# Kernel tuning notes

Measured on AMD Instinct MI355X. Metric: run time of the kernel, lower is better.

## Reference

```python
import jax, jax.numpy as jnp
import numpy as np

EPS = 1e-5

def conv3x3(x, w, b, stride=1):
    y = jax.lax.conv_general_dilated(x, w, (stride, stride), 'SAME',
                                     dimension_numbers=('NCHW', 'OIHW', 'NCHW'))
    return y + b[None, :, None, None]

def batchnorm_train(x, gamma, beta):
    # training-mode BN: batch statistics over (N, H, W)
    mean = x.mean(axis=(0, 2, 3), keepdims=True)
    var = x.var(axis=(0, 2, 3), keepdims=True)
    xh = (x - mean) * jax.lax.rsqrt(var + EPS)
    return xh * gamma[None, :, None, None] + beta[None, :, None, None]

def haar_dwt2(x):
    # pywt.dwt2(x, 'db1') on last two axes; even H,W so 'symmetric' padding is a no-op.
    # a = (x0 + x1)/sqrt2, d = (x0 - x1)/sqrt2 per axis -> 2x2 block combinations / 2.
    x00 = x[:, :, 0::2, 0::2]
    x01 = x[:, :, 0::2, 1::2]
    x10 = x[:, :, 1::2, 0::2]
    x11 = x[:, :, 1::2, 1::2]
    cA = (x00 + x01 + x10 + x11) * 0.5
    cH = (x00 + x01 - x10 - x11) * 0.5  # pywt 'da': detail along rows
    cV = (x00 - x01 + x10 - x11) * 0.5  # pywt 'ad': detail along cols
    cD = (x00 - x01 - x10 + x11) * 0.5
    return cA, cH, cV, cD


def setup_inputs() -> dict:
    key = jax.random.key(0)
    ks = jax.random.split(key, 8)
    N, in_c, out_c, H, W = 4, 3, 64, 512, 512

    def kaiming(k, shape):
        fan_in = shape[1] * shape[2] * shape[3]
        return jax.random.normal(k, shape, jnp.float32) * np.sqrt(2.0 / fan_in)

    inputs = jax.random.normal(ks[0], (N, in_c, H, W), jnp.float32)
    return {
        'inputs': inputs,
        # conv_block: conv1 -> bn1 -> conv2 -> bn2 -> relu
        'w1': kaiming(ks[1], (out_c, in_c, 3, 3)),
        'b1': jnp.zeros((out_c,), jnp.float32),
        'g1': jnp.ones((out_c,), jnp.float32),
        'be1': jnp.zeros((out_c,), jnp.float32),
        'w2': kaiming(ks[2], (out_c, out_c, 3, 3)),
        'b2': jnp.zeros((out_c,), jnp.float32),
        'g2': jnp.ones((out_c,), jnp.float32),
        'be2': jnp.zeros((out_c,), jnp.float32),
        # conv_dwt_block: conv(out_c*4 -> out_c) -> bn -> relu
        'w3': kaiming(ks[3], (out_c, out_c * 4, 3, 3)),
        'b3': jnp.zeros((out_c,), jnp.float32),
        'g3': jnp.ones((out_c,), jnp.float32),
        'be3': jnp.zeros((out_c,), jnp.float32),
    }


def reference(inputs, w1, b1, g1, be1, w2, b2, g2, be2, w3, b3, g3, be3):
    # conv_block
    x = conv3x3(inputs, w1, b1)
    x = batchnorm_train(x, g1, be1)
    x = conv3x3(x, w2, b2)
    x = batchnorm_train(x, g2, be2)
    skip_con = jax.nn.relu(x)

    # original detaches skip_con before the (CPU pywt) DWT -> no grad through this branch
    dwt_in = jax.lax.stop_gradient(skip_con)
    cA, cH, cV, cD = haar_dwt2(dwt_in)
    dwt = jnp.concatenate((cA, cH, cV, cD), axis=1)  # [N, 4*out_c, H/2, W/2]

    y = conv3x3(dwt, w3, b3)
    y = batchnorm_train(y, g3, be3)
    dwt_out = jax.nn.relu(y)
    return dwt_out, skip_con
```

## Files before the change

### kernel.cpp

```cpp
#include <hip/hip_runtime.h>
#include <cstdint>

typedef float f32x4 __attribute__((ext_vector_type(4)));
typedef __bf16 bf16x8 __attribute__((ext_vector_type(8)));
typedef unsigned int uint32;
typedef unsigned short ushort_t;

__device__ __forceinline__ ushort_t f2bf(float f) {
    uint32 u = __builtin_bit_cast(uint32, f);
    u = (u + 0x7fffu + ((u >> 16) & 1u)) >> 16;
    return (ushort_t)u;
}
__device__ __forceinline__ float bf2f(ushort_t h) {
    return __builtin_bit_cast(float, (uint32)h << 16);
}

__global__ __launch_bounds__(256) void im2col1_kernel(
    const float* __restrict__ in,
    ushort_t* __restrict__ P)
{
    int px = blockIdx.x * 256 + threadIdx.x;
    int n = px >> 18, rem = px & 262143;
    int y = rem >> 9, x = rem & 511;
    ushort_t pv[32];
#pragma unroll
    for (int ci = 0; ci < 3; ++ci)
#pragma unroll
        for (int t = 0; t < 9; ++t) {
            int dy = t / 3 - 1, dx = t % 3 - 1;
            int yy = y + dy, xx = x + dx;
            bool v = ((unsigned)yy < 512u) && ((unsigned)xx < 512u);
            pv[ci * 9 + t] = v ? f2bf(in[((n * 3 + ci) * 512 + yy) * 512 + xx])
                               : (ushort_t)0;
        }
#pragma unroll
    for (int k = 27; k < 32; ++k) pv[k] = 0;
    uint4* dst = (uint4*)(P + (size_t)px * 32);
    dst[0] = *(uint4*)(pv);
    dst[1] = *(uint4*)(pv + 8);
    dst[2] = *(uint4*)(pv + 16);
    dst[3] = *(uint4*)(pv + 24);
}

__global__ void prepw1_kernel(const float* __restrict__ w1,
                              ushort_t* __restrict__ Wsw1)
{
    int i = blockIdx.x * 256 + threadIdx.x;
    int ii = i & 7, lane = (i >> 3) & 63, nt = i >> 9;
    int cout = nt * 16 + (lane & 15);
    int k = (lane >> 4) * 8 + ii;
    Wsw1[i] = (k < 27) ? f2bf(w1[cout * 27 + k]) : (ushort_t)0;
}

__global__ __launch_bounds__(256) void gemm1_kernel(
    const ushort_t* __restrict__ P,
    const ushort_t* __restrict__ Wsw1,
    const float* __restrict__ b1,
    ushort_t* __restrict__ X1,
    float* __restrict__ stats)
{
    __shared__ float sred[4][128];
    int tid = threadIdx.x;
    int wave = tid >> 6, lane = tid & 63;
    int lp = lane & 15, lg = lane >> 4;
    int pxb = blockIdx.x * 256 + wave * 64;

    bf16x8 wf[4];
#pragma unroll
    for (int nt = 0; nt < 4; ++nt)
        wf[nt] = *(const bf16x8*)(Wsw1 + (nt * 64 + lane) * 8);

    f32x4 acc[4][4];
#pragma unroll
    for (int a = 0; a < 4; ++a)
#pragma unroll
        for (int b = 0; b < 4; ++b) acc[a][b] = (f32x4){0.f, 0.f, 0.f, 0.f};

#pragma unroll
    for (int nf = 0; nf < 4; ++nf) {
        bf16x8 bfrag = *(const bf16x8*)(P + (size_t)(pxb + nf * 16 + lp) * 32 + lg * 8);
#pragma unroll
        for (int nt = 0; nt < 4; ++nt)
            acc[nt][nf] = __builtin_amdgcn_mfma_f32_16x16x32_bf16(
                wf[nt], bfrag, acc[nt][nf], 0, 0, 0);
    }

    float s16[16], q16[16];
#pragma unroll
    for (int j = 0; j < 16; ++j) { s16[j] = 0.f; q16[j] = 0.f; }

#pragma unroll
    for (int nf = 0; nf < 4; ++nf) {
        size_t px = (size_t)pxb + nf * 16 + lp;
#pragma unroll
        for (int nt = 0; nt < 4; ++nt) {
            ushort_t ov[4];
#pragma unroll
            for (int r = 0; r < 4; ++r) {
                float o = acc[nt][nf][r] + b1[nt * 16 + lg * 4 + r];
                s16[nt * 4 + r] += o;
                q16[nt * 4 + r] += o * o;
                ov[r] = f2bf(o);
            }
            *(ushort4*)(X1 + px * 64 + nt * 16 + lg * 4) = *(ushort4*)ov;
        }
    }

#pragma unroll
    for (int off = 1; off < 16; off <<= 1)
#pragma unroll
        for (int j = 0; j < 16; ++j) {
            s16[j] += __shfl_xor(s16[j], off);
            q16[j] += __shfl_xor(q16[j], off);
        }
    if (lp == 0) {
#pragma unroll
        for (int nt = 0; nt < 4; ++nt)
#pragma unroll
            for (int r = 0; r < 4; ++r) {
                int ch = nt * 16 + lg * 4 + r;
                sred[wave][ch]      = s16[nt * 4 + r];
                sred[wave][64 + ch] = q16[nt * 4 + r];
            }
    }
    __syncthreads();
    if (tid < 128) {
        float tot = sred[0][tid] + sred[1][tid] + sred[2][tid] + sred[3][tid];
        atomicAdd(&stats[(blockIdx.x & 31) * 128 + tid], tot);
    }
}

__global__ void finalize_kernel(const float* __restrict__ stats,
                                const float* __restrict__ gamma,
                                const float* __restrict__ beta,
                                float inv_cnt, float* __restrict__ scsh)
{
    int c = threadIdx.x;
    float S = 0.f, Q = 0.f;
    for (int b = 0; b < 32; ++b) {
        S += stats[b * 128 + c];
        Q += stats[b * 128 + 64 + c];
    }
    float mean = S * inv_cnt;
    float var  = Q * inv_cnt - mean * mean;
    float rs   = rsqrtf(var + 1e-5f);
    float sc   = gamma[c] * rs;
    scsh[c]      = sc;
    scsh[64 + c] = beta[c] - mean * sc;
}

__global__ __launch_bounds__(256) void prepw_kernel(
    const float* __restrict__ w, const float* __restrict__ scale,
    ushort_t* __restrict__ Wsw, int CIN)
{
    int i = blockIdx.x * 256 + threadIdx.x;
    int KC = CIN >> 5;
    int ii = i & 7, lane = (i >> 3) & 63, nt = (i >> 9) & 3;
    int rest = i >> 11;
    int kc = rest % KC, t = rest / KC;
    if (t >= 9) return;
    int cout = nt * 16 + (lane & 15);
    int cin  = kc * 32 + (lane >> 4) * 8 + ii;
    float v = w[(cout * CIN + cin) * 9 + t];
    if (scale) v *= scale[cin];
    Wsw[i] = f2bf(v);
}

__global__ void prepT_kernel(const float* __restrict__ w2,
                             const float* __restrict__ shift,
                             float* __restrict__ T)
{
    int idx = threadIdx.x;
    if (idx < 576) {
        int t = idx / 64, cout = idx % 64;
        float s = 0.f;
        for (int cin = 0; cin < 64; ++cin)
            s += w2[(cout * 64 + cin) * 9 + t] * shift[cin];
        T[idx] = s;
    }
    __syncthreads();
    if (idx < 64) {
        float s = 0.f;
        for (int t = 0; t < 9; ++t) s += T[t * 64 + idx];
        T[576 + idx] = s;
    }
}

template <int CIN, bool HAS_T, int HH, int WW, int TILES>
__global__ __launch_bounds__(256, 3) void conv_mfma3_kernel(
    const ushort_t* __restrict__ X,
    const ushort_t* __restrict__ Wsw,
    const float* __restrict__ T,
    const float* __restrict__ bias,
    ushort_t* __restrict__ Y,
    float* __restrict__ stats)
{
    constexpr int KC     = CIN >> 5;
    constexpr int STAGES = TILES * KC;
    constexpr int CSTR   = WW / (64 * TILES);
    constexpr int RSTR   = HH >> 2;
    constexpr int NLD    = 1584;

    __shared__ ushort_t lds0[12672];
    __shared__ ushort_t lds1[12672];
    __shared__ float sred[4][128];

    int nwg = gridDim.x;
    int bid = blockIdx.x;
    int cpx = nwg >> 3;
    int bs  = (bid & 7) * cpx + (bid >> 3);

    int tid  = threadIdx.x;
    int wave = tid >> 6, lane = tid & 63;
    int lp = lane & 15, lg = lane >> 4;

    int tmp = bs;
    int cs = tmp % CSTR;  tmp /= CSTR;
    int rs = tmp % RSTR;
    int n  = tmp / RSTR;
    int y0 = rs << 2, x0 = cs * (64 * TILES);
    int y  = y0 + wave;

    for (int i = tid; i < 512; i += 256) ((float*)sred)[i] = 0.f;

    f32x4 acc[4][4];
#pragma unroll
    for (int a = 0; a < 4; ++a)
#pragma unroll
        for (int b = 0; b < 4; ++b) acc[a][b] = (f32x4){0.f, 0.f, 0.f, 0.f};

    uint4 rbuf[7];

    auto issue_stage = [&](int s) {
        int tj = s / KC, c = s - tj * KC;
        int xt = x0 + tj * 64;
#pragma unroll
        for (int j = 0; j < 7; ++j) {
            int idx = tid + j * 256;
            uint4 v = {0u, 0u, 0u, 0u};
            if (idx < NLD) {
                int p  = idx >> 2;
                int ry = p / 66, cx = p - ry * 66;
                int gy = y0 - 1 + ry, gx = xt - 1 + cx;
                if (((unsigned)gy < (unsigned)HH) && ((unsigned)gx < (unsigned)WW))
                    v = *(const uint4*)(X + ((size_t)(n * HH + gy) * WW + gx) * CIN
                                          + c * 32 + (idx & 3) * 8);
            }
            rbuf[j] = v;
        }
    };
    auto write_stage = [&](ushort_t* buf) {
#pragma unroll
        for (int j = 0; j < 7; ++j) {
            int idx = tid + j * 256;
            if (idx < NLD) ((uint4*)buf)[idx] = rbuf[j];
        }
    };

    issue_stage(0);
    write_stage(lds0);
    __syncthreads();

    ushort_t* cur = lds0;
    ushort_t* nxt = lds1;

#pragma unroll 1
    for (int s = 0; s < STAGES; ++s) {
        int tj = s / KC, c = s - tj * KC;
        if (s + 1 < STAGES) issue_stage(s + 1);

#pragma unroll
        for (int t = 0; t < 9; ++t) {
            const int dy = t / 3 - 1, dx = t % 3 - 1;
            bf16x8 wf[4];
#pragma unroll
            for (int nt = 0; nt < 4; ++nt)
                wf[nt] = *(const bf16x8*)(Wsw + (size_t)(((t * KC + c) << 2) + nt) * 512 + lane * 8);
            int prow = (wave + 1 + dy) * 66 + (1 + dx) + lp;
#pragma unroll
            for (int nf = 0; nf < 4; ++nf) {
                int px = prow + nf * 16;
                bf16x8 bfrag = *(const bf16x8*)((const char*)cur + px * 64 + lg * 16);
#pragma unroll
                for (int nt = 0; nt < 4; ++nt)
                    acc[nt][nf] = __builtin_amdgcn_mfma_f32_16x16x32_bf16(
                        wf[nt], bfrag, acc[nt][nf], 0, 0, 0);
            }
        }

        if (c == KC - 1) {
            int xt = x0 + tj * 64;
            bool top = (y == 0), bot = (y == HH - 1);
            float s16[16], q16[16];
            size_t rowbase = ((size_t)(n * HH + y) * WW) * 64;
#pragma unroll
            for (int nf = 0; nf < 4; ++nf) {
                int x = xt + nf * 16 + lp;
                bool lft = (x == 0), rgt = (x == WW - 1);
                bool edge = top | bot | lft | rgt;
#pragma unroll
                for (int nt = 0; nt < 4; ++nt) {
                    ushort_t ov[4];
#pragma unroll
                    for (int r = 0; r < 4; ++r) {
                        int ch = nt * 16 + lg * 4 + r;
                        float o = acc[nt][nf][r] + bias[ch];
                        if (HAS_T) {
                            o += T[576 + ch];
                            if (edge) {
#pragma unroll
                                for (int t = 0; t < 9; ++t) {
                                    int dy = t / 3 - 1, dx = t % 3 - 1;
                                    bool miss = (top && dy < 0) || (bot && dy > 0) ||
                                                (lft && dx < 0) || (rgt && dx > 0);
                                    if (miss) o -= T[t * 64 + ch];
                                }
                            }
                        }
                        if (nf == 0) { s16[nt * 4 + r] = o; q16[nt * 4 + r] = o * o; }
                        else         { s16[nt * 4 + r] += o; q16[nt * 4 + r] += o * o; }
                        ov[r] = f2bf(o);
                    }
                    *(ushort4*)(Y + rowbase + (size_t)x * 64 + nt * 16 + lg * 4) = *(ushort4*)ov;
                }
            }
#pragma unroll
            for (int off = 1; off < 16; off <<= 1)
#pragma unroll
                for (int j = 0; j < 16; ++j) {
                    s16[j] += __shfl_xor(s16[j], off);
                    q16[j] += __shfl_xor(q16[j], off);
                }
            if (lp == 0) {
#pragma unroll
                for (int nt = 0; nt < 4; ++nt)
#pragma unroll
                    for (int r = 0; r < 4; ++r) {
                        int ch = nt * 16 + lg * 4 + r;
                        sred[wave][ch]      += s16[nt * 4 + r];
                        sred[wave][64 + ch] += q16[nt * 4 + r];
                    }
            }
#pragma unroll
            for (int a = 0; a < 4; ++a)
#pragma unroll
                for (int b = 0; b < 4; ++b) acc[a][b] = (f32x4){0.f, 0.f, 0.f, 0.f};
        }

        if (s + 1 < STAGES) write_stage(nxt);
        __syncthreads();
        ushort_t* t2 = cur; cur = nxt; nxt = t2;
    }

    if (tid < 128) {
        float tot = sred[0][tid] + sred[1][tid] + sred[2][tid] + sred[3][tid];
        atomicAdd(&stats[(bs & 31) * 128 + tid], tot);
    }
}

__global__ __launch_bounds__(256) void bn2_dwt_skip_kernel(
    const ushort_t* __restrict__ X2, const float* __restrict__ scsh,
    float* __restrict__ skip,
    ushort_t* __restrict__ X3)
{
    __shared__ float v[128][65];
    int tid = threadIdx.x;
    int b = blockIdx.x;
    int n  = b >> 11;
    int r2 = b & 2047;
    int y0 = (r2 >> 3) << 1;
    int x0 = (r2 & 7) << 6;

#pragma unroll
    for (int k = 0; k < 4; ++k) {
        int q  = tid + k * 256;
        int px = q >> 3;
        int cb = (q & 7) * 8;
        int gy = y0 + (px >> 6);
        int gx = x0 + (px & 63);
        uint4 raw = *(const uint4*)(X2 + ((size_t)(n * 512 + gy) * 512 + gx) * 64 + cb);
        const ushort_t* up = (const ushort_t*)&raw;
#pragma unroll
        for (int j = 0; j < 8; ++j) {
            float f = bf2f(up[j]);
            float o = f * scsh[cb + j] + scsh[64 + cb + j];
            v[px][cb + j] = fmaxf(o, 0.f);
        }
    }
    __syncthreads();

    {
        int c = tid >> 2, sub = tid & 3;
#pragma unroll
        for (int rr = 0; rr < 2; ++rr) {
            float* orow = skip + ((size_t)(n * 64 + c) * 512 + (y0 + rr)) * 512 + x0;
#pragma unroll
            for (int qq = 0; qq < 4; ++qq) {
                int xb = qq * 16 + sub * 4;
                float4 w4;
                w4.x = v[rr * 64 + xb + 0][c];
                w4.y = v[rr * 64 + xb + 1][c];
                w4.z = v[rr * 64 + xb + 2][c];
                w4.w = v[rr * 64 + xb + 3][c];
                *(float4*)(orow + xb) = w4;
            }
        }
    }
    {
        int c = tid & 63, jj = tid >> 6;
        int yq = y0 >> 1, xq = x0 >> 1;
#pragma unroll
        for (int it = 0; it < 8; ++it) {
            int xl = jj * 8 + it;
            float x00 = v[2 * xl][c],      x01 = v[2 * xl + 1][c];
            float x10 = v[64 + 2 * xl][c], x11 = v[64 + 2 * xl + 1][c];
            float cA = (x00 + x01 + x10 + x11) * 0.5f;
            float cH = (x00 + x01 - x10 - x11) * 0.5f;
            float cV = (x00 - x01 + x10 - x11) * 0.5f;
            float cD = (x00 - x01 - x10 + x11) * 0.5f;
            ushort_t* dst = X3 + ((size_t)(n * 256 + yq) * 256 + xq + xl) * 256 + c;
            dst[0]   = f2bf(cA);
            dst[64]  = f2bf(cH);
            dst[128] = f2bf(cV);
            dst[192] = f2bf(cD);
        }
    }
}

__global__ __launch_bounds__(256) void bn3_kernel(
    const ushort_t* __restrict__ X4, const float* __restrict__ scsh,
    float* __restrict__ out)
{
    __shared__ float v[64][65];
    int tid = threadIdx.x;
    int b = blockIdx.x;
    int n  = b >> 10;
    int r2 = b & 1023;
    int y  = r2 >> 2;
    int x0 = (r2 & 3) << 6;

#pragma unroll
    for (int k = 0; k < 2; ++k) {
        int q  = tid + k * 256;
        int px = q >> 3;
        int cb = (q & 7) * 8;
        uint4 raw = *(const uint4*)(X4 + ((size_t)(n * 256 + y) * 256 + x0 + px) * 64 + cb);
        const ushort_t* up = (const ushort_t*)&raw;
#pragma unroll
        for (int j = 0; j < 8; ++j) {
            float f = bf2f(up[j]);
            float o = f * scsh[cb + j] + scsh[64 + cb + j];
            v[px][cb + j] = fmaxf(o, 0.f);
        }
    }
    __syncthreads();
    int c = tid >> 2, sub = tid & 3;
    float* orow = out + ((size_t)(n * 64 + c) * 256 + y) * 256 + x0;
#pragma unroll
    for (int qq = 0; qq < 4; ++qq) {
        int xb = qq * 16 + sub * 4;
        float4 w4;
        w4.x = v[xb + 0][c];
        w4.y = v[xb + 1][c];
        w4.z = v[xb + 2][c];
        w4.w = v[xb + 3][c];
        *(float4*)(orow + xb) = w4;
    }
}

extern "C" void kernel_launch(void* const* d_in, const int* in_sizes, int n_in,
                              void* d_out, int out_size, void* d_ws, size_t ws_size,
                              hipStream_t stream)
{
    const float* in  = (const float*)d_in[0];
    const float* w1  = (const float*)d_in[1];
    const float* b1  = (const float*)d_in[2];
    const float* g1  = (const float*)d_in[3];
    const float* be1 = (const float*)d_in[4];
    const float* w2  = (const float*)d_in[5];
    const float* b2  = (const float*)d_in[6];
    const float* g2  = (const float*)d_in[7];
    const float* be2 = (const float*)d_in[8];
    const float* w3  = (const float*)d_in[9];
    const float* b3  = (const float*)d_in[10];
    const float* g3  = (const float*)d_in[11];
    const float* be3 = (const float*)d_in[12];

    float* out     = (float*)d_out;
    float* dwt_out = out;
    float* skip    = out + 16777216;

    char* ws = (char*)d_ws;
    ushort_t* X1 = (ushort_t*)ws;
    ushort_t* X2 = (ushort_t*)(ws + 134217728);
    ushort_t* P  = X2;
    ushort_t* X3 = X1;
    ushort_t* X4 = X2;
    char* aux = ws + 268435456;
    float* stats1 = (float*)(aux);
    float* stats2 = (float*)(aux + 16384);
    float* stats3 = (float*)(aux + 32768);
    float* scsh1  = (float*)(aux + 49152);
    float* scsh2  = (float*)(aux + 49664);
    float* scsh3  = (float*)(aux + 50176);
    float* T2     = (float*)(aux + 50688);
    ushort_t* Wsw2 = (ushort_t*)(aux + 57344);
    ushort_t* Wsw3 = (ushort_t*)(aux + 131072);
    ushort_t* Wsw1 = (ushort_t*)(aux + 425984);

    hipMemsetAsync(aux, 0, 49152, stream);

    im2col1_kernel<<<4096, 256, 0, stream>>>(in, P);
    prepw1_kernel<<<8, 256, 0, stream>>>(w1, Wsw1);
    gemm1_kernel<<<4096, 256, 0, stream>>>(P, Wsw1, b1, X1, stats1);
    finalize_kernel<<<1, 64, 0, stream>>>(stats1, g1, be1, 1.f / 1048576.f, scsh1);
    prepw_kernel<<<144, 256, 0, stream>>>(w2, scsh1, Wsw2, 64);
    prepT_kernel<<<1, 576, 0, stream>>>(w2, scsh1 + 64, T2);

    conv_mfma3_kernel<64, true, 512, 512, 4><<<1024, 256, 0, stream>>>(
        X1, Wsw2, T2, b2, X2, stats2);
    finalize_kernel<<<1, 64, 0, stream>>>(stats2, g2, be2, 1.f / 1048576.f, scsh2);

    bn2_dwt_skip_kernel<<<8192, 256, 0, stream>>>(X2, scsh2, skip, X3);

    prepw_kernel<<<576, 256, 0, stream>>>(w3, nullptr, Wsw3, 256);
    conv_mfma3_kernel<256, false, 256, 256, 1><<<1024, 256, 0, stream>>>(
        X3, Wsw3, nullptr, b3, X4, stats3);
    finalize_kernel<<<1, 64, 0, stream>>>(stats3, g3, be3, 1.f / 262144.f, scsh3);

    bn3_kernel<<<4096, 256, 0, stream>>>(X4, scsh3, dwt_out);
}
```

Baseline: 620.5 us.

## Replace double-buffered multi-tile conv with single-buffer per-tile kernel

```diff
diff --git a/kernel.cpp b/kernel.cpp
--- a/kernel.cpp
+++ b/kernel.cpp
@@ -186,8 +186,8 @@
     }
 }
 
-template <int CIN, bool HAS_T, int HH, int WW, int TILES>
-__global__ __launch_bounds__(256, 3) void conv_mfma3_kernel(
+template <int CIN, bool HAS_T, int HH, int WW>
+__global__ __launch_bounds__(256, 4) void conv_mfma4_kernel(
     const ushort_t* __restrict__ X,
     const ushort_t* __restrict__ Wsw,
     const float* __restrict__ T,
@@ -196,13 +196,10 @@
     float* __restrict__ stats)
 {
     constexpr int KC     = CIN >> 5;
-    constexpr int STAGES = TILES * KC;
-    constexpr int CSTR   = WW / (64 * TILES);
-    constexpr int RSTR   = HH >> 2;
-    constexpr int NLD    = 1584;
-
-    __shared__ ushort_t lds0[12672];
-    __shared__ ushort_t lds1[12672];
+    constexpr int COLS_B = WW >> 6;
+    constexpr int ROWS_B = HH >> 2;
+
+    __shared__ ushort_t tile[12672];
     __shared__ float sred[4][128];
 
     int nwg = gridDim.x;
@@ -215,59 +212,36 @@
     int lp = lane & 15, lg = lane >> 4;
 
     int tmp = bs;
-    int cs = tmp % CSTR;  tmp /= CSTR;
-    int rs = tmp % RSTR;
-    int n  = tmp / RSTR;
-    int y0 = rs << 2, x0 = cs * (64 * TILES);
+    int ctile = tmp % COLS_B;  tmp /= COLS_B;
+    int rtile = tmp % ROWS_B;
+    int n     = tmp / ROWS_B;
+    int y0 = rtile << 2, x0 = ctile << 6;
     int y  = y0 + wave;
 
-    for (int i = tid; i < 512; i += 256) ((float*)sred)[i] = 0.f;
-
     f32x4 acc[4][4];
 #pragma unroll
     for (int a = 0; a < 4; ++a)
 #pragma unroll
         for (int b = 0; b < 4; ++b) acc[a][b] = (f32x4){0.f, 0.f, 0.f, 0.f};
 
-    uint4 rbuf[7];
-
-    auto issue_stage = [&](int s) {
-        int tj = s / KC, c = s - tj * KC;
-        int xt = x0 + tj * 64;
+#pragma unroll 1
+    for (int c = 0; c < KC; ++c) {
+        if (c) __syncthreads();
 #pragma unroll
         for (int j = 0; j < 7; ++j) {
-            int idx = tid + j * 256;
-            uint4 v = {0u, 0u, 0u, 0u};
-            if (idx < NLD) {
-                int p  = idx >> 2;
-                int ry = p / 66, cx = p - ry * 66;
-                int gy = y0 - 1 + ry, gx = xt - 1 + cx;
+            int s = tid + j * 256;
+            if (s < 1584) {
+                int px = s >> 2, cb = s & 3;
+                int ry = px / 66, cx = px - ry * 66;
+                int gy = y0 - 1 + ry, gx = x0 - 1 + cx;
+                uint4 v = {0u, 0u, 0u, 0u};
                 if (((unsigned)gy < (unsigned)HH) && ((unsigned)gx < (unsigned)WW))
                     v = *(const uint4*)(X + ((size_t)(n * HH + gy) * WW + gx) * CIN
-                                          + c * 32 + (idx & 3) * 8);
-            }
-            rbuf[j] = v;
-        }
-    };
-    auto write_stage = [&](ushort_t* buf) {
-#pragma unroll
-        for (int j = 0; j < 7; ++j) {
-            int idx = tid + j * 256;
-            if (idx < NLD) ((uint4*)buf)[idx] = rbuf[j];
-        }
-    };
-
-    issue_stage(0);
-    write_stage(lds0);
-    __syncthreads();
-
-    ushort_t* cur = lds0;
-    ushort_t* nxt = lds1;
-
-#pragma unroll 1
-    for (int s = 0; s < STAGES; ++s) {
-        int tj = s / KC, c = s - tj * KC;
-        if (s + 1 < STAGES) issue_stage(s + 1);
+                                          + c * 32 + cb * 8);
+                *(uint4*)(tile + cb * 3168 + px * 8) = v;
+            }
+        }
+        __syncthreads();
 
 #pragma unroll
         for (int t = 0; t < 9; ++t) {
@@ -280,78 +254,71 @@
 #pragma unroll
             for (int nf = 0; nf < 4; ++nf) {
                 int px = prow + nf * 16;
-                bf16x8 bfrag = *(const bf16x8*)((const char*)cur + px * 64 + lg * 16);
+                bf16x8 bfrag = *(const bf16x8*)(tile + lg * 3168 + px * 8);
 #pragma unroll
                 for (int nt = 0; nt < 4; ++nt)
                     acc[nt][nf] = __builtin_amdgcn_mfma_f32_16x16x32_bf16(
                         wf[nt], bfrag, acc[nt][nf], 0, 0, 0);
             }
         }
-
-        if (c == KC - 1) {
-            int xt = x0 + tj * 64;
-            bool top = (y == 0), bot = (y == HH - 1);
-            float s16[16], q16[16];
-            size_t rowbase = ((size_t)(n * HH + y) * WW) * 64;
-#pragma unroll
-            for (int nf = 0; nf < 4; ++nf) {
-                int x = xt + nf * 16 + lp;
-                bool lft = (x == 0), rgt = (x == WW - 1);
-                bool edge = top | bot | lft | rgt;
-#pragma unroll
-                for (int nt = 0; nt < 4; ++nt) {
-                    ushort_t ov[4];
-#pragma unroll
-                    for (int r = 0; r < 4; ++r) {
-                        int ch = nt * 16 + lg * 4 + r;
-                        float o = acc[nt][nf][r] + bias[ch];
-                        if (HAS_T) {
-                            o += T[576 + ch];
-                            if (edge) {
-#pragma unroll
-                                for (int t = 0; t < 9; ++t) {
-                                    int dy = t / 3 - 1, dx = t % 3 - 1;
-                                    bool miss = (top && dy < 0) || (bot && dy > 0) ||
-                                                (lft && dx < 0) || (rgt && dx > 0);
-                                    if (miss) o -= T[t * 64 + ch];
-                                }
-                            }
+    }
+
+    bool top = (y == 0), bot = (y == HH - 1);
+    float s16[16], q16[16];
+#pragma unroll
+    for (int j = 0; j < 16; ++j) { s16[j] = 0.f; q16[j] = 0.f; }
+
+    size_t rowbase = ((size_t)(n * HH + y) * WW) * 64;
+#pragma unroll
+    for (int nf = 0; nf < 4; ++nf) {
+        int x = x0 + nf * 16 + lp;
+        bool lft = (x == 0), rgt = (x == WW - 1);
+        bool edge = top | bot | lft | rgt;
+#pragma unroll
+        for (int nt = 0; nt < 4; ++nt) {
+            ushort_t ov[4];
+#pragma unroll
+            for (int r = 0; r < 4; ++r) {
+                int ch = nt * 16 + lg * 4 + r;
+                float o = acc[nt][nf][r] + bias[ch];
+                if (HAS_T) {
+                    o += T[576 + ch];
+                    if (edge) {
+#pragma unroll
+                        for (int t = 0; t < 9; ++t) {
+                            int dy = t / 3 - 1, dx = t % 3 - 1;
+                            bool miss = (top && dy < 0) || (bot && dy > 0) ||
+                                        (lft && dx < 0) || (rgt && dx > 0);
+                            if (miss) o -= T[t * 64 + ch];
                         }
-                        if (nf == 0) { s16[nt * 4 + r] = o; q16[nt * 4 + r] = o * o; }
-                        else         { s16[nt * 4 + r] += o; q16[nt * 4 + r] += o * o; }
-                        ov[r] = f2bf(o);
                     }
-                    *(ushort4*)(Y + rowbase + (size_t)x * 64 + nt * 16 + lg * 4) = *(ushort4*)ov;
                 }
-            }
-#pragma unroll
-            for (int off = 1; off < 16; off <<= 1)
-#pragma unroll
-                for (int j = 0; j < 16; ++j) {
-                    s16[j] += __shfl_xor(s16[j], off);
-                    q16[j] += __shfl_xor(q16[j], off);
-                }
-            if (lp == 0) {
-#pragma unroll
-                for (int nt = 0; nt < 4; ++nt)
-#pragma unroll
-                    for (int r = 0; r < 4; ++r) {
-                        int ch = nt * 16 + lg * 4 + r;
-                        sred[wave][ch]      += s16[nt * 4 + r];
-                        sred[wave][64 + ch] += q16[nt * 4 + r];
-                    }
-            }
-#pragma unroll
-            for (int a = 0; a < 4; ++a)
-#pragma unroll
-                for (int b = 0; b < 4; ++b) acc[a][b] = (f32x4){0.f, 0.f, 0.f, 0.f};
-        }
-
-        if (s + 1 < STAGES) write_stage(nxt);
-        __syncthreads();
-        ushort_t* t2 = cur; cur = nxt; nxt = t2;
-    }
-
+                s16[nt * 4 + r] += o;
+                q16[nt * 4 + r] += o * o;
+                ov[r] = f2bf(o);
+            }
+            *(ushort4*)(Y + rowbase + (size_t)x * 64 + nt * 16 + lg * 4) = *(ushort4*)ov;
+        }
+    }
+
+#pragma unroll
+    for (int off = 1; off < 16; off <<= 1)
+#pragma unroll
+        for (int j = 0; j < 16; ++j) {
+            s16[j] += __shfl_xor(s16[j], off);
+            q16[j] += __shfl_xor(q16[j], off);
+        }
+    if (lp == 0) {
+#pragma unroll
+        for (int nt = 0; nt < 4; ++nt)
+#pragma unroll
+            for (int r = 0; r < 4; ++r) {
+                int ch = nt * 16 + lg * 4 + r;
+                sred[wave][ch]      = s16[nt * 4 + r];
+                sred[wave][64 + ch] = q16[nt * 4 + r];
+            }
+    }
+    __syncthreads();
     if (tid < 128) {
         float tot = sred[0][tid] + sred[1][tid] + sred[2][tid] + sred[3][tid];
         atomicAdd(&stats[(bs & 31) * 128 + tid], tot);
@@ -517,14 +484,14 @@
     prepw_kernel<<<144, 256, 0, stream>>>(w2, scsh1, Wsw2, 64);
     prepT_kernel<<<1, 576, 0, stream>>>(w2, scsh1 + 64, T2);
 
-    conv_mfma3_kernel<64, true, 512, 512, 4><<<1024, 256, 0, stream>>>(
+    conv_mfma4_kernel<64, true, 512, 512><<<4096, 256, 0, stream>>>(
         X1, Wsw2, T2, b2, X2, stats2);
     finalize_kernel<<<1, 64, 0, stream>>>(stats2, g2, be2, 1.f / 1048576.f, scsh2);
 
     bn2_dwt_skip_kernel<<<8192, 256, 0, stream>>>(X2, scsh2, skip, X3);
 
     prepw_kernel<<<576, 256, 0, stream>>>(w3, nullptr, Wsw3, 256);
-    conv_mfma3_kernel<256, false, 256, 256, 1><<<1024, 256, 0, stream>>>(
+    conv_mfma4_kernel<256, false, 256, 256><<<1024, 256, 0, stream>>>(
         X3, Wsw3, nullptr, b3, X4, stats3);
     finalize_kernel<<<1, 64, 0, stream>>>(stats3, g3, be3, 1.f / 262144.f, scsh3);
 
```

Measured after the change: 552.9 us. -10.9%, faster.
